# Kernel optimization log

Measured on AMD Instinct MI355X. Metric: run time of the kernel, lower is better.

## Reference

```python
import jax, jax.numpy as jnp
import numpy as np

EMB = 256   # EMB_SIZE hard-coded in source
H = 8       # num heads (all heads share the same Q/K/V, as in source)
DK = EMB // H  # 32
B, T = 16, 2048
LN_EPS = 1e-5


def _layernorm(a, g, b):
    m = jnp.mean(a, axis=-1, keepdims=True)
    v = jnp.mean(jnp.square(a - m), axis=-1, keepdims=True)
    return (a - m) * jax.lax.rsqrt(v + LN_EPS) * g + b


def setup_inputs() -> dict:
    key = jax.random.key(0)
    ks = jax.random.split(key, 8)
    sc = 0.02
    return {
        "x": jax.random.normal(ks[0], (B, T, EMB), jnp.float32),
        "Wq": jax.random.normal(ks[1], (EMB, DK), jnp.float32) * sc,
        "Wk": jax.random.normal(ks[2], (EMB, DK), jnp.float32) * sc,
        "Wv": jax.random.normal(ks[3], (EMB, DK), jnp.float32) * sc,
        "Wp": jax.random.normal(ks[4], (EMB, EMB), jnp.float32) * sc,
        "bp": jnp.zeros((EMB,), jnp.float32),
        "W1": jax.random.normal(ks[5], (EMB, 4 * EMB), jnp.float32) * sc,
        "b1": jnp.zeros((4 * EMB,), jnp.float32),
        "W2": jax.random.normal(ks[6], (4 * EMB, EMB), jnp.float32) * sc,
        "b2": jnp.zeros((EMB,), jnp.float32),
        "g1": jnp.ones((EMB,), jnp.float32),
        "be1": jnp.zeros((EMB,), jnp.float32),
        "g2": jnp.ones((EMB,), jnp.float32),
        "be2": jnp.zeros((EMB,), jnp.float32),
    }


def reference(x, Wq, Wk, Wv, Wp, bp, W1, b1, W2, b2, g1, be1, g2, be2):
    # Single shared-head QKV projections (bias-free), as in source
    q = x @ Wq  # [B,T,DK]
    k = x @ Wk
    v = x @ Wv
    # Causal self-attention with explicit score matrix [B,T,T]
    scores = jnp.einsum("btd,bsd->bts", q, k) / jnp.sqrt(jnp.float32(DK))
    causal = jnp.tril(jnp.ones((T, T), dtype=bool))
    scores = jnp.where(causal, scores, -jnp.inf)
    a = jax.nn.softmax(scores, axis=-1)
    attn = jnp.einsum("bts,bsd->btd", a, v)  # [B,T,DK]
    # Source concatenates h identical copies of the same attention output
    cat = jnp.tile(attn, (1, 1, H))  # [B,T,EMB]
    mh = cat @ Wp + bp
    y1 = _layernorm(x + mh, g1, be1)
    ff = jax.nn.gelu(y1 @ W1 + b1, approximate=False) @ W2 + b2
    return _layernorm(y1 + ff, g2, be2)
```

## Files before the change

### kernel.cpp

```cpp
#include <hip/hip_runtime.h>

#define BB 16
#define TT 2048
#define EE 256
#define DK 32
#define MM (BB*TT)
#define FF 1024

typedef __bf16 bf16_t;
typedef __bf16 bf16x8 __attribute__((ext_vector_type(8)));
typedef __bf16 bf16x4 __attribute__((ext_vector_type(4)));
typedef float  f32x4  __attribute__((ext_vector_type(4)));

__device__ __forceinline__ f32x4 mfma16(bf16x8 a, bf16x8 b, f32x4 c){
  return __builtin_amdgcn_mfma_f32_16x16x32_bf16(a, b, c, 0, 0, 0);
}
__device__ __forceinline__ void gload_lds16(const void* g, void* l){
  __builtin_amdgcn_global_load_lds((__attribute__((address_space(1))) void*)g,
                                   (__attribute__((address_space(3))) void*)l,
                                   16, 0, 0);
}

__launch_bounds__(256)
__global__ void prep_kernel(const float* __restrict__ Wq, const float* __restrict__ Wk,
                            const float* __restrict__ Wv, const float* __restrict__ Wp,
                            const float* __restrict__ W1, const float* __restrict__ W2,
                            bf16_t* __restrict__ wqkv, float* __restrict__ wpe,
                            bf16_t* __restrict__ w1t, bf16_t* __restrict__ w2t)
{
  const int i = blockIdx.x*256 + threadIdx.x;
  if (i < 96*256) {
    const int r = i >> 8, c = i & 255;
    float v;
    if (r < 32)      v = Wq[c*32 + r] * 0.17677669529663687f;
    else if (r < 64) v = Wk[c*32 + (r-32)];
    else             v = Wv[c*32 + (r-64)];
    wqkv[i] = (bf16_t)v;
  }
  if (i < 32*256) {
    const int d = i >> 8, n = i & 255;
    float s = 0.f;
    #pragma unroll
    for (int h = 0; h < 8; ++h) s += Wp[(h*32 + d)*256 + n];
    wpe[i] = s;
  }
  if (i < 1024*256) {
    const int n = i >> 8, k = i & 255;
    w1t[i] = (bf16_t)W1[(size_t)k*1024 + n];
  }
  if (i < 256*1024) {
    const int n = i >> 10, k = i & 1023;
    w2t[i] = (bf16_t)W2[(size_t)k*256 + n];
  }
}

__launch_bounds__(256)
__global__ void qkv_kernel(const float* __restrict__ x, const bf16_t* __restrict__ wqkv,
                           bf16_t* __restrict__ q, bf16_t* __restrict__ kd,
                           bf16_t* __restrict__ vT)
{
  __shared__ bf16_t Ws[96*256];
  bf16_t* Vt = Ws;
  const int tid = threadIdx.x;
  #pragma unroll
  for (int i = 0; i < 12; ++i) {
    const int v8  = tid + i*256;
    const int row = v8 >> 5;
    const int bir = (v8 & 31) * 16;
    *(bf16x8*)((char*)Ws + row*512 + (bir ^ ((row & 7) << 4))) =
        *(const bf16x8*)(wqkv + (size_t)v8*8);
  }
  __syncthreads();

  const int w = tid >> 6, l = tid & 63;
  const int lr = l & 15, lk4 = l >> 4, lkb = lk4*8;
  const int m0 = blockIdx.x * 64;
  const int arow = m0 + w*16 + lr;
  const float* xr = x + (size_t)arow * 256;

  f32x4 acc[6] = {};
  #pragma unroll
  for (int s = 0; s < 8; ++s) {
    const int kb = s*32 + lkb;
    const float4 v0 = *(const float4*)(xr + kb);
    const float4 v1 = *(const float4*)(xr + kb + 4);
    bf16x8 a;
    a[0]=(bf16_t)v0.x; a[1]=(bf16_t)v0.y; a[2]=(bf16_t)v0.z; a[3]=(bf16_t)v0.w;
    a[4]=(bf16_t)v1.x; a[5]=(bf16_t)v1.y; a[6]=(bf16_t)v1.z; a[7]=(bf16_t)v1.w;
    #pragma unroll
    for (int j = 0; j < 6; ++j) {
      const int nrow = j*16 + lr;
      const bf16x8 bf = *(const bf16x8*)((const char*)Ws + nrow*512 +
                                         ((kb*2) ^ ((nrow & 7) << 4)));
      acc[j] = mfma16(a, bf, acc[j]);
    }
  }
  #pragma unroll
  for (int j = 0; j < 4; ++j) {
    #pragma unroll
    for (int r = 0; r < 4; ++r) {
      const int orow = m0 + w*16 + lk4*4 + r;
      const int col  = j*16 + lr;
      const bf16_t v = (bf16_t)acc[j][r];
      if (col < 32) q[(size_t)orow*32 + col] = v;
      else          kd[(size_t)orow*32 + (col-32)] = v;
    }
  }
  __syncthreads();
  #pragma unroll
  for (int j = 4; j < 6; ++j)
    #pragma unroll
    for (int r = 0; r < 4; ++r) {
      const int d = (j-4)*16 + lr;
      const int t = w*16 + lk4*4 + r;
      *(bf16_t*)((char*)Vt + d*128 + ((((t>>3) ^ (d&7))<<4) | ((t&7)*2))) =
          (bf16_t)acc[j][r];
    }
  __syncthreads();
  {
    const int d = tid >> 3, c8 = tid & 7;
    const bf16x8 v = *(const bf16x8*)((char*)Vt + d*128 + ((c8 ^ (d&7))<<4));
    *(bf16x8*)(vT + ((size_t)(m0 >> 11)*32 + d)*TT + (m0 & 2047) + c8*8) = v;
  }
}

__launch_bounds__(256)
__global__ void attnp_kernel(const bf16_t* __restrict__ q, const bf16_t* __restrict__ kd,
                             const bf16_t* __restrict__ vT,
                             float* __restrict__ part_acc, float* __restrict__ part_ml)
{
  __shared__ bf16_t P[4][16*128];
  const int tid = threadIdx.x;
  const int w = tid >> 6, l = tid & 63;
  const int wv = blockIdx.x*4 + w;
  const int lr = l & 15, g4 = l >> 4;
  const float NEG_INF = -__builtin_inff();

  const int b = wv / 320;
  const int u = wv - b*320;
  int r, base;
  if      (u >= 192) { r = 3; base = 192; }
  else if (u >= 96)  { r = 2; base = 96;  }
  else if (u >= 32)  { r = 1; base = 32;  }
  else               { r = 0; base = 0;   }
  const int qq = u - base;
  const int g  = r*32 + qq / (r+1);
  const int c  = qq - (qq / (r+1))*(r+1);
  const int t_total = (g >> 3) + 1;
  const int t0 = c*4;
  const int t1 = min(t0 + 4, t_total);

  const bf16_t* qb = q  + (size_t)b*TT*32;
  const bf16_t* kb = kd + (size_t)b*TT*32;
  const bf16_t* vb = vT + (size_t)b*32*TT;
  const int q0 = g*16;
  const int qg = q0 + lr;

  const bf16x8 qa = *(const bf16x8*)(qb + (size_t)(q0 + lr)*32 + g4*8);
  const bf16_t* v0r = vb + (size_t)lr*TT;
  const bf16_t* v1r = vb + (size_t)(16 + lr)*TT;

  f32x4 acc0 = {0.f,0.f,0.f,0.f}, acc1 = {0.f,0.f,0.f,0.f};
  float mrun = NEG_INF, lsum = 0.f;
  char* pb = (char*)&P[w][0];
  const int swz = (lr & 7) << 4;
  const f32x4 zf = {0.f,0.f,0.f,0.f};

  for (int t = t0; t < t1; ++t) {
    const int k0 = t * 128;
    f32x4 s[8];
    #pragma unroll
    for (int cc = 0; cc < 8; ++cc) {
      const bf16x8 kf = *(const bf16x8*)(kb + (size_t)(k0 + cc*16 + lr)*32 + g4*8);
      s[cc] = mfma16(kf, qa, zf);
    }
    if (t == t_total - 1) {
      #pragma unroll
      for (int cc = 0; cc < 8; ++cc)
        #pragma unroll
        for (int rr = 0; rr < 4; ++rr)
          if (k0 + cc*16 + g4*4 + rr > qg) s[cc][rr] = NEG_INF;
    }
    float mt = NEG_INF;
    #pragma unroll
    for (int cc = 0; cc < 8; ++cc) {
      float a01 = fmaxf(s[cc][0], s[cc][1]), a23 = fmaxf(s[cc][2], s[cc][3]);
      mt = fmaxf(mt, fmaxf(a01, a23));
    }
    mt = fmaxf(mt, __shfl_xor(mt, 16));
    mt = fmaxf(mt, __shfl_xor(mt, 32));
    const float mn = fmaxf(mrun, mt);
    const float sc = __expf(mrun - mn);
    float ps = 0.f;
    #pragma unroll
    for (int cc = 0; cc < 8; ++cc) {
      float p0 = __expf(s[cc][0]-mn), p1 = __expf(s[cc][1]-mn);
      float p2 = __expf(s[cc][2]-mn), p3 = __expf(s[cc][3]-mn);
      s[cc][0]=p0; s[cc][1]=p1; s[cc][2]=p2; s[cc][3]=p3;
      ps += (p0+p1) + (p2+p3);
    }
    ps += __shfl_xor(ps, 16);
    ps += __shfl_xor(ps, 32);
    lsum = lsum*sc + ps;
    mrun = mn;
    acc0 *= sc; acc1 *= sc;
    #pragma unroll
    for (int cc = 0; cc < 8; ++cc) {
      bf16x4 pk;
      pk[0]=(bf16_t)s[cc][0]; pk[1]=(bf16_t)s[cc][1];
      pk[2]=(bf16_t)s[cc][2]; pk[3]=(bf16_t)s[cc][3];
      *(bf16x4*)(pb + lr*256 + ((cc*32 + g4*8) ^ swz)) = pk;
    }
    #pragma unroll
    for (int h = 0; h < 4; ++h) {
      const bf16x8 pbf = *(const bf16x8*)(pb + lr*256 + ((h*64 + g4*16) ^ swz));
      acc0 = mfma16(*(const bf16x8*)(v0r + k0 + h*32 + g4*8), pbf, acc0);
      acc1 = mfma16(*(const bf16x8*)(v1r + k0 + h*32 + g4*8), pbf, acc1);
    }
  }
  float* pa = part_acc + (size_t)wv*512;
  *(f32x4*)(pa + l*8)     = acc0;
  *(f32x4*)(pa + l*8 + 4) = acc1;
  if (l < 16) {
    part_ml[wv*32 + l]      = mrun;
    part_ml[wv*32 + 16 + l] = lsum;
  }
}

__launch_bounds__(256)
__global__ void attnc_kernel(const float* __restrict__ part_acc,
                             const float* __restrict__ part_ml,
                             bf16_t* __restrict__ attn)
{
  const int tid = threadIdx.x;
  const int id = blockIdx.x*4 + (tid >> 6);
  const int l = tid & 63, lr = l & 15, g4 = l >> 4;
  const int b = id >> 7, g = id & 127;
  const int r = g >> 5;
  const int base = (r == 0) ? 0 : (r == 1) ? 32 : (r == 2) ? 96 : 192;
  const int p0 = b*320 + base + (g - (r << 5))*(r + 1);
  const int nc = r + 1;
  const float NEG_INF = -__builtin_inff();

  float m0v=NEG_INF,m1v=NEG_INF,m2v=NEG_INF,m3v=NEG_INF;
  float l0v=0,l1v=0,l2v=0,l3v=0;
  f32x4 a00={0,0,0,0},a01={0,0,0,0},a10={0,0,0,0},a11={0,0,0,0};
  f32x4 a20={0,0,0,0},a21={0,0,0,0},a30={0,0,0,0},a31={0,0,0,0};
  {
    const float* pa = part_acc + (size_t)p0*512;
    a00 = *(const f32x4*)(pa + l*8); a01 = *(const f32x4*)(pa + l*8 + 4);
    m0v = part_ml[p0*32 + lr]; l0v = part_ml[p0*32 + 16 + lr];
  }
  if (nc > 1) {
    const float* pa = part_acc + (size_t)(p0+1)*512;
    a10 = *(const f32x4*)(pa + l*8); a11 = *(const f32x4*)(pa + l*8 + 4);
    m1v = part_ml[(p0+1)*32 + lr]; l1v = part_ml[(p0+1)*32 + 16 + lr];
  }
  if (nc > 2) {
    const float* pa = part_acc + (size_t)(p0+2)*512;
    a20 = *(const f32x4*)(pa + l*8); a21 = *(const f32x4*)(pa + l*8 + 4);
    m2v = part_ml[(p0+2)*32 + lr]; l2v = part_ml[(p0+2)*32 + 16 + lr];
  }
  if (nc > 3) {
    const float* pa = part_acc + (size_t)(p0+3)*512;
    a30 = *(const f32x4*)(pa + l*8); a31 = *(const f32x4*)(pa + l*8 + 4);
    m3v = part_ml[(p0+3)*32 + lr]; l3v = part_ml[(p0+3)*32 + 16 + lr];
  }
  const float M = fmaxf(fmaxf(m0v, m1v), fmaxf(m2v, m3v));
  const float w0 = __expf(m0v - M), w1 = __expf(m1v - M);
  const float w2 = __expf(m2v - M), w3 = __expf(m3v - M);
  const float L = l0v*w0 + l1v*w1 + l2v*w2 + l3v*w3;
  const float inv = 1.0f / L;
  f32x4 o0 = (a00*w0 + a10*w1 + a20*w2 + a30*w3) * inv;
  f32x4 o1 = (a01*w0 + a11*w1 + a21*w2 + a31*w3) * inv;

  bf16_t* ao = attn + ((size_t)b*TT + g*16 + lr)*32;
  bf16x4 ob0, ob1;
  ob0[0]=(bf16_t)o0[0]; ob0[1]=(bf16_t)o0[1]; ob0[2]=(bf16_t)o0[2]; ob0[3]=(bf16_t)o0[3];
  ob1[0]=(bf16_t)o1[0]; ob1[1]=(bf16_t)o1[1]; ob1[2]=(bf16_t)o1[2]; ob1[3]=(bf16_t)o1[3];
  *(bf16x4*)(ao + g4*4)      = ob0;
  *(bf16x4*)(ao + 16 + g4*4) = ob1;
}

__launch_bounds__(256)
__global__ void ln1_kernel(const float* __restrict__ x, const bf16_t* __restrict__ attn,
                           const float* __restrict__ wpe, const float* __restrict__ bp,
                           const float* __restrict__ g1, const float* __restrict__ be1,
                           bf16_t* __restrict__ y1b)
{
  __shared__ float Wp_s[32*256];
  const int tid = threadIdx.x;
  for (int i = tid; i < 32*64; i += 256)
    ((float4*)Wp_s)[i] = ((const float4*)wpe)[i];
  __syncthreads();

  const int w = tid >> 6, l = tid & 63;
  const int n = l * 4;
  const float4 gv  = *(const float4*)(g1  + n);
  const float4 bev = *(const float4*)(be1 + n);
  const float4 bpv = *(const float4*)(bp  + n);

  #pragma unroll 1
  for (int it = 0; it < 8; ++it) {
    const int row = blockIdx.x*32 + it*4 + w;
    const bf16_t* ar = attn + (size_t)row*32;
    float a[32];
    #pragma unroll
    for (int i = 0; i < 4; ++i) {
      const bf16x8 t = *(const bf16x8*)(ar + i*8);
      #pragma unroll
      for (int j = 0; j < 8; ++j) a[i*8 + j] = (float)t[j];
    }
    float mh[4] = {bpv.x, bpv.y, bpv.z, bpv.w};
    #pragma unroll
    for (int d = 0; d < 32; ++d) {
      const float4 wv = *(const float4*)(Wp_s + d*256 + n);
      const float ad = a[d];
      mh[0] = fmaf(ad, wv.x, mh[0]); mh[1] = fmaf(ad, wv.y, mh[1]);
      mh[2] = fmaf(ad, wv.z, mh[2]); mh[3] = fmaf(ad, wv.w, mh[3]);
    }
    const float4 xv = *(const float4*)(x + (size_t)row*256 + n);
    const float t0 = xv.x + mh[0], t1 = xv.y + mh[1];
    const float t2 = xv.z + mh[2], t3 = xv.w + mh[3];
    float s1 = (t0+t1) + (t2+t3);
    float s2 = (t0*t0 + t1*t1) + (t2*t2 + t3*t3);
    #pragma unroll
    for (int m = 1; m < 64; m <<= 1) { s1 += __shfl_xor(s1, m); s2 += __shfl_xor(s2, m); }
    const float mean = s1 * (1.0f/256.0f);
    const float var  = s2 * (1.0f/256.0f) - mean*mean;
    const float rs   = rsqrtf(var + 1e-5f);
    float4 yv;
    yv.x = (t0-mean)*rs*gv.x + bev.x; yv.y = (t1-mean)*rs*gv.y + bev.y;
    yv.z = (t2-mean)*rs*gv.z + bev.z; yv.w = (t3-mean)*rs*gv.w + bev.w;
    bf16x4 yb; yb[0]=(bf16_t)yv.x; yb[1]=(bf16_t)yv.y; yb[2]=(bf16_t)yv.z; yb[3]=(bf16_t)yv.w;
    *(bf16x4*)(y1b + (size_t)row*256 + n) = yb;
  }
}

__launch_bounds__(512, 1)
__global__ void mlp_kernel(const bf16_t* __restrict__ y1b, const bf16_t* __restrict__ w1t,
                           const float* __restrict__ b1, const bf16_t* __restrict__ w2t,
                           const float* __restrict__ b2, const float* __restrict__ g2,
                           const float* __restrict__ be2, float* __restrict__ out)
{
  __shared__ char SM[151552];
  const int tid = threadIdx.x;
  const int w = tid >> 6, l = tid & 63;
  const int lr = l & 15, g4 = l >> 4;
  const int m0 = blockIdx.x * 128;
  const int rw = w & 3;
  const int cw = w >> 2;
  const int wm  = rw * 32;
  const int wn1 = cw * 32;
  const int wn2 = cw * 128;

  {
    const float2 bv = *(const float2*)(b1 + tid*2);
    *(float2*)(SM + 147456 + tid*8) = bv;
  }

  bf16x8 aA[2][8];
  #pragma unroll
  for (int t = 0; t < 2; ++t)
    #pragma unroll
    for (int kk = 0; kk < 8; ++kk)
      aA[t][kk] = *(const bf16x8*)(y1b +
          (size_t)(m0 + wm + t*16 + lr)*256 + kk*32 + g4*8);
  asm volatile("s_waitcnt vmcnt(0) lgkmcnt(0)" ::: "memory");
  __builtin_amdgcn_sched_barrier(0);

  #define ST_W1(i, d)                                                         \
    { _Pragma("unroll")                                                       \
      for (int p_ = 0; p_ < 4; ++p_) {                                        \
        const int idx_ = p_*512 + tid;                                        \
        const int r_ = idx_ >> 5, c_ = idx_ & 31;                             \
        const int sc_ = (c_ & 24) | ((c_ ^ r_) & 7);                          \
        gload_lds16(w1t + (size_t)((i)*64 + r_)*256 + sc_*8,                  \
                    SM + (d)*32768 + idx_*16);                                \
      } }
  #define ST_W2(i, d)                                                         \
    { _Pragma("unroll")                                                       \
      for (int p_ = 0; p_ < 4; ++p_) {                                        \
        const int idx_ = p_*512 + tid;                                        \
        const int r_ = idx_ >> 3, c_ = idx_ & 7;                              \
        gload_lds16(w2t + (size_t)r_*1024 + (i)*64 + ((c_ ^ r_) & 7)*8,       \
                    SM + 65536 + (d)*32768 + idx_*16);                        \
      } }

  ST_W1(0, 0);
  ST_W2(0, 0);
  ST_W1(1, 1);

  f32x4 oacc[2][8] = {};
  char* hb = SM + 131072;

  #pragma unroll 1
  for (int i = 0; i < 16; ++i) {
    if (i < 15) { asm volatile("s_waitcnt vmcnt(8)" ::: "memory"); }
    else        { asm volatile("s_waitcnt vmcnt(4)" ::: "memory"); }
    __builtin_amdgcn_sched_barrier(0);
    __builtin_amdgcn_s_barrier();
    const char* sw1 = SM + (i & 1)*32768;
    f32x4 ah[2][2] = {};
    __builtin_amdgcn_s_setprio(1);
    #pragma unroll
    for (int kk = 0; kk < 8; ++kk) {
      const int off = kk*64 + g4*16;
      const int n0r = wn1 + lr, n1r = wn1 + 16 + lr;
      const bf16x8 bf0 = *(const bf16x8*)(sw1 + n0r*512 + (off ^ ((n0r & 7) << 4)));
      const bf16x8 bf1 = *(const bf16x8*)(sw1 + n1r*512 + (off ^ ((n1r & 7) << 4)));
      ah[0][0] = mfma16(aA[0][kk], bf0, ah[0][0]);
      ah[0][1] = mfma16(aA[0][kk], bf1, ah[0][1]);
      ah[1][0] = mfma16(aA[1][kk], bf0, ah[1][0]);
      ah[1][1] = mfma16(aA[1][kk], bf1, ah[1][1]);
    }
    __builtin_amdgcn_s_setprio(0);
    #pragma unroll
    for (int j = 0; j < 2; ++j) {
      const float bias = *(const float*)(SM + 147456 + (i*64 + wn1 + j*16 + lr)*4);
      const int hcol2 = (wn1 + j*16 + lr)*2;
      #pragma unroll
      for (int t = 0; t < 2; ++t)
        #pragma unroll
        for (int r = 0; r < 4; ++r) {
          const int hrow = wm + t*16 + g4*4 + r;
          const float v = ah[t][j][r] + bias;
          const float z = 1.5957691216057308f * v * fmaf(0.044715f, v*v, 1.0f);
          const float gg = v * __builtin_amdgcn_rcpf(1.0f + __expf(-z));
          *(bf16_t*)(hb + hrow*128 + (hcol2 ^ ((hrow & 7) << 4))) = (bf16_t)gg;
        }
    }
    asm volatile("s_waitcnt lgkmcnt(0)" ::: "memory");
    __builtin_amdgcn_sched_barrier(0);
    if (i < 15) { asm volatile("s_waitcnt vmcnt(4)" ::: "memory"); }
    else        { asm volatile("s_waitcnt vmcnt(0)" ::: "memory"); }
    __builtin_amdgcn_sched_barrier(0);
    __builtin_amdgcn_s_barrier();
    const char* sw2 = SM + 65536 + (i & 1)*32768;
    __builtin_amdgcn_s_setprio(1);
    #pragma unroll
    for (int kk2 = 0; kk2 < 2; ++kk2) {
      const int off = kk2*64 + g4*16;
      bf16x8 ha[2], wb[8];
      #pragma unroll
      for (int i3 = 0; i3 < 2; ++i3) {
        const int row = wm + i3*16 + lr;
        ha[i3] = *(const bf16x8*)(hb + row*128 + (off ^ ((row & 7) << 4)));
      }
      #pragma unroll
      for (int j3 = 0; j3 < 8; ++j3) {
        const int n = wn2 + j3*16 + lr;
        wb[j3] = *(const bf16x8*)(sw2 + n*128 + (off ^ ((n & 7) << 4)));
      }
      #pragma unroll
      for (int i3 = 0; i3 < 2; ++i3)
        #pragma unroll
        for (int j3 = 0; j3 < 8; ++j3)
          oacc[i3][j3] = mfma16(ha[i3], wb[j3], oacc[i3][j3]);
    }
    __builtin_amdgcn_s_setprio(0);
    if (i < 15) ST_W2(i+1, (i+1)&1);
    if (i < 14) ST_W1(i+2, i&1);
  }
  #undef ST_W1
  #undef ST_W2

  float b2r[8], g2r[8], be2r[8];
  #pragma unroll
  for (int j3 = 0; j3 < 8; ++j3) {
    const int col = wn2 + j3*16 + lr;
    b2r[j3] = b2[col]; g2r[j3] = g2[col]; be2r[j3] = be2[col];
  }
  #pragma unroll
  for (int i3 = 0; i3 < 2; ++i3)
    #pragma unroll
    for (int r = 0; r < 4; ++r) {
      const int grow = m0 + wm + i3*16 + g4*4 + r;
      #pragma unroll
      for (int j3 = 0; j3 < 8; ++j3) {
        const int col = wn2 + j3*16 + lr;
        oacc[i3][j3][r] += b2r[j3] + (float)y1b[(size_t)grow*256 + col];
      }
    }
  __syncthreads();
  float* red = (float*)SM;
  #pragma unroll
  for (int i3 = 0; i3 < 2; ++i3)
    #pragma unroll
    for (int r = 0; r < 4; ++r) {
      float s1 = 0.f, s2 = 0.f;
      #pragma unroll
      for (int j3 = 0; j3 < 8; ++j3) {
        s1 += oacc[i3][j3][r]; s2 += oacc[i3][j3][r]*oacc[i3][j3][r];
      }
      #pragma unroll
      for (int m = 1; m < 16; m <<= 1) { s1 += __shfl_xor(s1, m); s2 += __shfl_xor(s2, m); }
      if (lr == 0) {
        const int rl = wm + i3*16 + g4*4 + r;
        red[rl*4 + cw*2]     = s1;
        red[rl*4 + cw*2 + 1] = s2;
      }
    }
  __syncthreads();
  #pragma unroll
  for (int i3 = 0; i3 < 2; ++i3)
    #pragma unroll
    for (int r = 0; r < 4; ++r) {
      const int rl = wm + i3*16 + g4*4 + r;
      const float S1 = red[rl*4+0] + red[rl*4+2];
      const float S2 = red[rl*4+1] + red[rl*4+3];
      const float mean = S1 * (1.0f/256.0f);
      const float var  = S2 * (1.0f/256.0f) - mean*mean;
      const float rs   = rsqrtf(var + 1e-5f);
      #pragma unroll
      for (int j3 = 0; j3 < 8; ++j3) {
        const int col = wn2 + j3*16 + lr;
        out[(size_t)(m0 + rl)*256 + col] = (oacc[i3][j3][r] - mean)*rs*g2r[j3] + be2r[j3];
      }
    }
}

extern "C" void kernel_launch(void* const* d_in, const int* in_sizes, int n_in,
                              void* d_out, int out_size, void* d_ws, size_t ws_size,
                              hipStream_t stream)
{
  const float* x   = (const float*)d_in[0];
  const float* Wq  = (const float*)d_in[1];
  const float* Wk  = (const float*)d_in[2];
  const float* Wv  = (const float*)d_in[3];
  const float* Wp  = (const float*)d_in[4];
  const float* bp  = (const float*)d_in[5];
  const float* W1  = (const float*)d_in[6];
  const float* b1  = (const float*)d_in[7];
  const float* W2  = (const float*)d_in[8];
  const float* b2  = (const float*)d_in[9];
  const float* g1  = (const float*)d_in[10];
  const float* be1 = (const float*)d_in[11];
  const float* g2  = (const float*)d_in[12];
  const float* be2 = (const float*)d_in[13];

  char* ws = (char*)d_ws;
  bf16_t* qd   = (bf16_t*)(ws + ((size_t)0  << 20));
  bf16_t* kd   = (bf16_t*)(ws + ((size_t)2  << 20));
  bf16_t* vTd  = (bf16_t*)(ws + ((size_t)4  << 20));
  bf16_t* attn = (bf16_t*)(ws + ((size_t)6  << 20));
  bf16_t* y1b  = (bf16_t*)(ws + ((size_t)8  << 20));
  bf16_t* wqkv = (bf16_t*)(ws + ((size_t)24 << 20));
  float*  wpe  = (float*) (ws + ((size_t)25 << 20));
  bf16_t* w1t  = (bf16_t*)(ws + ((size_t)26 << 20));
  bf16_t* w2t  = (bf16_t*)(ws + ((size_t)27 << 20));
  float*  pml  = (float*) (ws + ((size_t)28 << 20));
  float*  pacc = (float*) (ws + ((size_t)29 << 20));
  float* out = (float*)d_out;

  prep_kernel<<<1024, 256, 0, stream>>>(Wq, Wk, Wv, Wp, W1, W2, wqkv, wpe, w1t, w2t);
  qkv_kernel<<<512, 256, 0, stream>>>(x, wqkv, qd, kd, vTd);
  attnp_kernel<<<1280, 256, 0, stream>>>(qd, kd, vTd, pacc, pml);
  attnc_kernel<<<512, 256, 0, stream>>>(pacc, pml, attn);
  ln1_kernel<<<1024, 256, 0, stream>>>(x, attn, wpe, bp, g1, be1, y1b);
  mlp_kernel<<<256, 512, 0, stream>>>(y1b, w1t, b1, w2t, b2, g2, be2, out);
}
```

Before: 128.0 us.

## Software-pipeline MLP kernel with 32-wide hidden chunks and triple-buffered weights

Halves the hidden-dimension chunk in the fused MLP kernel from 64 to 32 and doubles the iteration count. Weight tiles now sit in three LDS buffers and the GELU output in a double buffer. Each iteration runs GEMM1 for chunk i and GEMM2 for chunk i-1, which cuts the barriers per iteration from two to one and lets the first GEMM overlap the second. The price is more loop iterations with smaller MFMA batches, an epilogue GEMM2 step, and slightly less LDS.

Measured after the change: 133.2 us. +4.1%, slower.

```diff
diff --git a/kernel.cpp b/kernel.cpp
--- a/kernel.cpp
+++ b/kernel.cpp
@@ -343,7 +343,7 @@
                            const float* __restrict__ b2, const float* __restrict__ g2,
                            const float* __restrict__ be2, float* __restrict__ out)
 {
-  __shared__ char SM[151552];
+  __shared__ char SM[135168];
   const int tid = threadIdx.x;
   const int w = tid >> 6, l = tid & 63;
   const int lr = l & 15, g4 = l >> 4;
@@ -351,14 +351,13 @@
   const int rw = w & 3;
   const int cw = w >> 2;
   const int wm  = rw * 32;
-  const int wn1 = cw * 32;
+  const int wn1 = cw * 16;
   const int wn2 = cw * 128;
 
   {
     const float2 bv = *(const float2*)(b1 + tid*2);
-    *(float2*)(SM + 147456 + tid*8) = bv;
-  }
-
+    *(float2*)(SM + 131072 + tid*8) = bv;
+  }
   bf16x8 aA[2][8];
   #pragma unroll
   for (int t = 0; t < 2; ++t)
@@ -369,88 +368,64 @@
   asm volatile("s_waitcnt vmcnt(0) lgkmcnt(0)" ::: "memory");
   __builtin_amdgcn_sched_barrier(0);
 
-  #define ST_W1(i, d)                                                         \
+  #define ST_W1(c, s)                                                         \
     { _Pragma("unroll")                                                       \
-      for (int p_ = 0; p_ < 4; ++p_) {                                        \
+      for (int p_ = 0; p_ < 2; ++p_) {                                        \
         const int idx_ = p_*512 + tid;                                        \
         const int r_ = idx_ >> 5, c_ = idx_ & 31;                             \
         const int sc_ = (c_ & 24) | ((c_ ^ r_) & 7);                          \
-        gload_lds16(w1t + (size_t)((i)*64 + r_)*256 + sc_*8,                  \
-                    SM + (d)*32768 + idx_*16);                                \
+        gload_lds16(w1t + (size_t)((c)*32 + r_)*256 + sc_*8,                  \
+                    SM + (s)*16384 + idx_*16);                                \
       } }
-  #define ST_W2(i, d)                                                         \
+  #define ST_W2(c, s)                                                         \
     { _Pragma("unroll")                                                       \
-      for (int p_ = 0; p_ < 4; ++p_) {                                        \
+      for (int p_ = 0; p_ < 2; ++p_) {                                        \
         const int idx_ = p_*512 + tid;                                        \
-        const int r_ = idx_ >> 3, c_ = idx_ & 7;                              \
-        gload_lds16(w2t + (size_t)r_*1024 + (i)*64 + ((c_ ^ r_) & 7)*8,       \
-                    SM + 65536 + (d)*32768 + idx_*16);                        \
+        const int r_ = idx_ >> 2, c_ = idx_ & 3;                              \
+        gload_lds16(w2t + (size_t)r_*1024 + (c)*32 + ((c_ ^ r_) & 3)*8,       \
+                    SM + 49152 + (s)*16384 + idx_*16);                        \
       } }
 
   ST_W1(0, 0);
+  ST_W1(1, 1);
   ST_W2(0, 0);
-  ST_W1(1, 1);
 
   f32x4 oacc[2][8] = {};
-  char* hb = SM + 131072;
 
   #pragma unroll 1
-  for (int i = 0; i < 16; ++i) {
-    if (i < 15) { asm volatile("s_waitcnt vmcnt(8)" ::: "memory"); }
-    else        { asm volatile("s_waitcnt vmcnt(4)" ::: "memory"); }
+  for (int i = 0; i < 32; ++i) {
+    if (i < 31) { asm volatile("s_waitcnt vmcnt(4)" ::: "memory"); }
+    else        { asm volatile("s_waitcnt vmcnt(2)" ::: "memory"); }
+    __builtin_amdgcn_sched_barrier(0);
+    asm volatile("s_waitcnt lgkmcnt(0)" ::: "memory");
     __builtin_amdgcn_sched_barrier(0);
     __builtin_amdgcn_s_barrier();
-    const char* sw1 = SM + (i & 1)*32768;
-    f32x4 ah[2][2] = {};
+    __builtin_amdgcn_sched_barrier(0);
+
+    const char* sw1 = SM + (i % 3)*16384;
+    f32x4 ah[2] = {};
+    const int nr = wn1 + lr;
     __builtin_amdgcn_s_setprio(1);
     #pragma unroll
     for (int kk = 0; kk < 8; ++kk) {
-      const int off = kk*64 + g4*16;
-      const int n0r = wn1 + lr, n1r = wn1 + 16 + lr;
-      const bf16x8 bf0 = *(const bf16x8*)(sw1 + n0r*512 + (off ^ ((n0r & 7) << 4)));
-      const bf16x8 bf1 = *(const bf16x8*)(sw1 + n1r*512 + (off ^ ((n1r & 7) << 4)));
-      ah[0][0] = mfma16(aA[0][kk], bf0, ah[0][0]);
-      ah[0][1] = mfma16(aA[0][kk], bf1, ah[0][1]);
-      ah[1][0] = mfma16(aA[1][kk], bf0, ah[1][0]);
-      ah[1][1] = mfma16(aA[1][kk], bf1, ah[1][1]);
-    }
-    __builtin_amdgcn_s_setprio(0);
-    #pragma unroll
-    for (int j = 0; j < 2; ++j) {
-      const float bias = *(const float*)(SM + 147456 + (i*64 + wn1 + j*16 + lr)*4);
-      const int hcol2 = (wn1 + j*16 + lr)*2;
-      #pragma unroll
-      for (int t = 0; t < 2; ++t)
-        #pragma unroll
-        for (int r = 0; r < 4; ++r) {
-          const int hrow = wm + t*16 + g4*4 + r;
-          const float v = ah[t][j][r] + bias;
-          const float z = 1.5957691216057308f * v * fmaf(0.044715f, v*v, 1.0f);
-          const float gg = v * __builtin_amdgcn_rcpf(1.0f + __expf(-z));
-          *(bf16_t*)(hb + hrow*128 + (hcol2 ^ ((hrow & 7) << 4))) = (bf16_t)gg;
-        }
-    }
-    asm volatile("s_waitcnt lgkmcnt(0)" ::: "memory");
-    __builtin_amdgcn_sched_barrier(0);
-    if (i < 15) { asm volatile("s_waitcnt vmcnt(4)" ::: "memory"); }
-    else        { asm volatile("s_waitcnt vmcnt(0)" ::: "memory"); }
-    __builtin_amdgcn_sched_barrier(0);
-    __builtin_amdgcn_s_barrier();
-    const char* sw2 = SM + 65536 + (i & 1)*32768;
-    __builtin_amdgcn_s_setprio(1);
-    #pragma unroll
-    for (int kk2 = 0; kk2 < 2; ++kk2) {
-      const int off = kk2*64 + g4*16;
+      const bf16x8 bf = *(const bf16x8*)(sw1 + nr*512 +
+                                         ((kk*64 + g4*16) ^ ((nr & 7) << 4)));
+      ah[0] = mfma16(aA[0][kk], bf, ah[0]);
+      ah[1] = mfma16(aA[1][kk], bf, ah[1]);
+    }
+    if (i > 0) {
+      const char* sw2 = SM + 49152 + ((i-1) % 3)*16384;
+      const char* hs  = SM + 98304 + ((i-1) & 1)*16384;
       bf16x8 ha[2], wb[8];
       #pragma unroll
       for (int i3 = 0; i3 < 2; ++i3) {
         const int row = wm + i3*16 + lr;
-        ha[i3] = *(const bf16x8*)(hb + row*128 + (off ^ ((row & 7) << 4)));
+        ha[i3] = *(const bf16x8*)(hs + row*128 + ((g4*16) ^ ((row & 7) << 4)));
       }
       #pragma unroll
       for (int j3 = 0; j3 < 8; ++j3) {
         const int n = wn2 + j3*16 + lr;
-        wb[j3] = *(const bf16x8*)(sw2 + n*128 + (off ^ ((n & 7) << 4)));
+        wb[j3] = *(const bf16x8*)(sw2 + n*64 + ((g4*16) ^ ((n & 3) << 4)));
       }
       #pragma unroll
       for (int i3 = 0; i3 < 2; ++i3)
@@ -459,11 +434,53 @@
           oacc[i3][j3] = mfma16(ha[i3], wb[j3], oacc[i3][j3]);
     }
     __builtin_amdgcn_s_setprio(0);
-    if (i < 15) ST_W2(i+1, (i+1)&1);
-    if (i < 14) ST_W1(i+2, i&1);
+    {
+      const float bias = *(const float*)(SM + 131072 + (i*32 + wn1 + lr)*4);
+      char* hw = SM + 98304 + (i & 1)*16384;
+      const int hc2 = (wn1 + lr)*2;
+      #pragma unroll
+      for (int i3 = 0; i3 < 2; ++i3)
+        #pragma unroll
+        for (int r = 0; r < 4; ++r) {
+          const int hrow = wm + i3*16 + g4*4 + r;
+          const float v = ah[i3][r] + bias;
+          const float z = 1.5957691216057308f * v * fmaf(0.044715f, v*v, 1.0f);
+          const float gg = v * __builtin_amdgcn_rcpf(1.0f + __expf(-z));
+          *(bf16_t*)(hw + hrow*128 + (hc2 ^ ((hrow & 7) << 4))) = (bf16_t)gg;
+        }
+    }
+    if (i <= 29) ST_W1(i+2, (i+2) % 3);
+    if (i <= 30) ST_W2(i+1, (i+1) % 3);
   }
   #undef ST_W1
   #undef ST_W2
+
+  asm volatile("s_waitcnt vmcnt(0)" ::: "memory");
+  __builtin_amdgcn_sched_barrier(0);
+  asm volatile("s_waitcnt lgkmcnt(0)" ::: "memory");
+  __builtin_amdgcn_sched_barrier(0);
+  __builtin_amdgcn_s_barrier();
+  __builtin_amdgcn_sched_barrier(0);
+  {
+    const char* sw2 = SM + 49152 + (31 % 3)*16384;
+    const char* hs  = SM + 98304 + (31 & 1)*16384;
+    bf16x8 ha[2], wb[8];
+    #pragma unroll
+    for (int i3 = 0; i3 < 2; ++i3) {
+      const int row = wm + i3*16 + lr;
+      ha[i3] = *(const bf16x8*)(hs + row*128 + ((g4*16) ^ ((row & 7) << 4)));
+    }
+    #pragma unroll
+    for (int j3 = 0; j3 < 8; ++j3) {
+      const int n = wn2 + j3*16 + lr;
+      wb[j3] = *(const bf16x8*)(sw2 + n*64 + ((g4*16) ^ ((n & 3) << 4)));
+    }
+    #pragma unroll
+    for (int i3 = 0; i3 < 2; ++i3)
+      #pragma unroll
+      for (int j3 = 0; j3 < 8; ++j3)
+        oacc[i3][j3] = mfma16(ha[i3], wb[j3], oacc[i3][j3]);
+  }
 
   float b2r[8], g2r[8], be2r[8];
   #pragma unroll
```
